# Kernel tuning notes

Hardware: AMD Instinct MI355X
Metric: run time of the kernel (lower is better)

The kernel has to match this reference:

```python
import jax, jax.numpy as jnp
import numpy as np

D_MODEL = 512
NHEAD = 8
D_HEAD = D_MODEL // NHEAD
SCALE = D_HEAD ** -0.5
EPS = 1e-8


def setup_inputs() -> dict:
    key = jax.random.key(0)
    ks = jax.random.split(key, 12)
    B, N = 4, 2048
    s = D_MODEL ** -0.5
    return {
        "Q_input": jax.random.normal(ks[0], (B, N, D_MODEL), jnp.float32),
        "KV_input": jax.random.normal(ks[1], (B, N, D_MODEL), jnp.float32),
        "SC": jax.random.uniform(ks[2], (B, N, N), jnp.float32),
        "Wq_w": jax.random.normal(ks[3], (D_MODEL, D_MODEL), jnp.float32) * s,
        "Wq_b": jnp.zeros((D_MODEL,), jnp.float32),
        "Wk_w": jax.random.normal(ks[4], (D_MODEL, D_MODEL), jnp.float32) * s,
        "Wk_b": jnp.zeros((D_MODEL,), jnp.float32),
        "Wv_w": jax.random.normal(ks[5], (D_MODEL, D_MODEL), jnp.float32) * s,
        "Wv_b": jnp.zeros((D_MODEL,), jnp.float32),
        "gate_w": jax.random.normal(ks[6], (), jnp.float32),
        "gate_b": jnp.zeros((), jnp.float32),
        "out_w": jax.random.normal(ks[7], (D_MODEL, D_MODEL), jnp.float32) * s,
        "out_b": jnp.zeros((D_MODEL,), jnp.float32),
    }


def reference(Q_input, KV_input, SC, Wq_w, Wq_b, Wk_w, Wk_b, Wv_w, Wv_b,
              gate_w, gate_b, out_w, out_b):
    B, N, _ = Q_input.shape
    # projections -> [B, H, N, d_head]
    def proj(x, w, b):
        y = x @ w.T + b
        return y.reshape(B, N, NHEAD, D_HEAD).transpose(0, 2, 1, 3)
    Q = proj(Q_input, Wq_w, Wq_b)
    K = proj(KV_input, Wk_w, Wk_b)
    V = proj(KV_input, Wv_w, Wv_b)
    # scores [B, H, N, N]
    scores = jnp.einsum('bhqd,bhkd->bhqk', Q, K) * SCALE
    # per-edge gate: sigmoid(w*SC + b), broadcast over heads
    g = jax.nn.sigmoid(SC * gate_w + gate_b)  # [B, N, N]
    scores = scores + jnp.log(g + EPS)[:, None, :, :]
    attn = jax.nn.softmax(scores, axis=-1)
    out = jnp.einsum('bhqk,bhkd->bhqd', attn, V)
    out = out.transpose(0, 2, 1, 3).reshape(B, N, D_MODEL)
    return out @ out_w.T + out_b
```

## Files before the change

kernel.cpp:

```cpp
#include <hip/hip_runtime.h>

typedef unsigned short u16;
typedef unsigned int u32;
typedef __attribute__((ext_vector_type(4))) float f32x4;
typedef __attribute__((ext_vector_type(8))) short s16x8;
typedef __attribute__((ext_vector_type(4))) u16 u16x4;

#define L2E 1.4426950408889634f
#define QSCALE 0.18033688011112042f

__device__ __forceinline__ float bf2f(u16 u) {
    union { u32 i; float f; } v; v.i = ((u32)u) << 16; return v.f;
}
__device__ __forceinline__ u16 f2bf(float f) {
    union { float f; u32 i; } v; v.f = f;
    return (u16)((v.i + 0x7fffu + ((v.i >> 16) & 1u)) >> 16);
}
__device__ __forceinline__ u32 pack_hi(float a, float b) {
    union { float f; u32 i; } x, y; x.f = a; y.f = b;
    return (x.i >> 16) | (y.i & 0xFFFF0000u);
}

__device__ __forceinline__ void gl2lds16(const u16* g, u16* l) {
    __builtin_amdgcn_global_load_lds(
        (const __attribute__((address_space(1))) void*)g,
        (__attribute__((address_space(3))) void*)l, 16, 0, 0);
}

__global__ __launch_bounds__(256) void prep_kernel(
    const float* __restrict__ s0, const float* __restrict__ s1,
    const float* __restrict__ s2, const float* __restrict__ s3,
    const float* __restrict__ s4, const float* __restrict__ s5,
    u16* __restrict__ dst,
    const float* __restrict__ SC, const float* __restrict__ gwp,
    const float* __restrict__ gbp, u16* __restrict__ LGx)
{
    if (blockIdx.x < 9216) {
        int e = (blockIdx.x * 256 + threadIdx.x) * 4;
        const float* src; int off;
        if      (e < 4194304) { src = s0; off = e; }
        else if (e < 8388608) { src = s1; off = e - 4194304; }
        else if (e < 8650752) { src = s2; off = e - 8388608; }
        else if (e < 8912896) { src = s3; off = e - 8650752; }
        else if (e < 9175040) { src = s4; off = e - 8912896; }
        else                  { src = s5; off = e - 9175040; }
        f32x4 f = *(const f32x4*)(src + off);
        u16x4 o;
#pragma unroll
        for (int j = 0; j < 4; ++j) o[j] = f2bf(f[j]);
        *(u16x4*)(dst + e) = o;
    } else {
        const int flat = (blockIdx.x - 9216) * 256 + threadIdx.x;
        const int lane = flat & 63;
        const int kt   = (flat >> 6) & 31;
        const int t16  = (flat >> 11) & 127;
        const int b    = flat >> 18;
        const int l16 = lane & 15, quad = lane >> 4;
        const float tA = -gwp[0] * L2E, tB = -gbp[0] * L2E;
        const float* row = SC + ((size_t)b * 2048 + t16 * 16 + l16) * 2048
                              + kt * 64 + quad * 4;
        __align__(16) u16 tmp[16];
#pragma unroll
        for (int kk = 0; kk < 4; ++kk) {
            f32x4 x = *(const f32x4*)(row + kk * 16);
#pragma unroll
            for (int reg = 0; reg < 4; ++reg) {
                float g = __builtin_amdgcn_rcpf(
                    1.0f + __builtin_amdgcn_exp2f(tA * x[reg] + tB)) + 1e-8f;
                tmp[kk * 4 + reg] = f2bf(__builtin_amdgcn_logf(g));
            }
        }
        u16* d = LGx + (size_t)flat * 16;
        *(uint4*)d       = *(uint4*)tmp;
        *(uint4*)(d + 8) = *(uint4*)(tmp + 8);
    }
}

__device__ __forceinline__ void gemm_core(
    const u16* __restrict__ A, const u16* __restrict__ Bw,
    int m0, int n0, u16* As, u16* Bs, f32x4 acc[4][4])
{
    const int tid = threadIdx.x;
    const int lane = tid & 63, w = tid >> 6;
    const int wm = w >> 1, wn = w & 1;
    const int l16 = lane & 15, quad = lane >> 4;
    const int srow = (lane >> 2), sch = (lane & 3) * 8;
    const f32x4 vzero = {0.f, 0.f, 0.f, 0.f};
#pragma unroll
    for (int i = 0; i < 4; ++i)
#pragma unroll
        for (int j = 0; j < 4; ++j) acc[i][j] = vzero;

#pragma unroll
    for (int j = 0; j < 2; ++j) {
        int row = w * 32 + j * 16 + srow;
        gl2lds16(&A[(size_t)(m0 + row) * 512 + sch], &As[w * 1024 + j * 512]);
        gl2lds16(&Bw[(size_t)(n0 + row) * 512 + sch], &Bs[w * 1024 + j * 512]);
    }
    for (int kt = 0; kt < 16; ++kt) {
        __syncthreads();
        const int cur = (kt & 1) * 4096;
        if (kt < 15) {
            const int nxt = ((kt + 1) & 1) * 4096;
#pragma unroll
            for (int j = 0; j < 2; ++j) {
                int row = w * 32 + j * 16 + srow;
                gl2lds16(&A[(size_t)(m0 + row) * 512 + (kt + 1) * 32 + sch],
                         &As[nxt + w * 1024 + j * 512]);
                gl2lds16(&Bw[(size_t)(n0 + row) * 512 + (kt + 1) * 32 + sch],
                         &Bs[nxt + w * 1024 + j * 512]);
            }
        }
        s16x8 af[4], bfr[4];
#pragma unroll
        for (int mt = 0; mt < 4; ++mt)
            af[mt] = *(const s16x8*)&As[cur + (wm * 64 + mt * 16 + l16) * 32 + quad * 8];
#pragma unroll
        for (int nt = 0; nt < 4; ++nt)
            bfr[nt] = *(const s16x8*)&Bs[cur + (wn * 64 + nt * 16 + l16) * 32 + quad * 8];
#pragma unroll
        for (int mt = 0; mt < 4; ++mt)
#pragma unroll
            for (int nt = 0; nt < 4; ++nt)
                acc[mt][nt] = __builtin_amdgcn_mfma_f32_16x16x32_bf16(
                    af[mt], bfr[nt], acc[mt][nt], 0, 0, 0);
    }
}

__global__ __launch_bounds__(256) void proj_kernel(
    const u16* __restrict__ cQin, const u16* __restrict__ cKV,
    const u16* __restrict__ cW,
    const float* __restrict__ bq, const float* __restrict__ bk,
    const float* __restrict__ bv,
    u16* __restrict__ Qh, u16* __restrict__ Kh, u16* __restrict__ Vt)
{
    __shared__ __align__(16) u16 As[2 * 4096];
    __shared__ __align__(16) u16 Bs[2 * 4096];
    const int job = blockIdx.z;
    const u16* A = (job == 0) ? cQin : cKV;
    const u16* W = cW + (size_t)job * 262144;
    const float* bias = (job == 0) ? bq : (job == 1 ? bk : bv);
    const int m0 = blockIdx.y * 128, n0 = blockIdx.x * 128;
    f32x4 acc[4][4];
    gemm_core(A, W, m0, n0, As, Bs, acc);

    const int tid = threadIdx.x, lane = tid & 63, w = tid >> 6;
    const int wm = w >> 1, wn = w & 1, l16 = lane & 15, quad = lane >> 4;
#pragma unroll
    for (int nt = 0; nt < 4; ++nt) {
        int j = n0 + wn * 64 + nt * 16 + l16;
        float bj = bias[j];
        int h = j >> 6, d = j & 63;
#pragma unroll
        for (int mt = 0; mt < 4; ++mt) {
            int trow = m0 + wm * 64 + mt * 16 + quad * 4;
            int bb = trow >> 11, nn = trow & 2047;
            int bh = bb * 8 + h;
            if (job == 2) {
                u16x4 pv;
#pragma unroll
                for (int reg = 0; reg < 4; ++reg) pv[reg] = f2bf(acc[mt][nt][reg] + bj);
                *(u16x4*)&Vt[(size_t)(bh * 64 + d) * 2048 + nn] = pv;
            } else if (job == 0) {
#pragma unroll
                for (int reg = 0; reg < 4; ++reg)
                    Qh[(size_t)(bh * 2048 + nn + reg) * 64 + d] =
                        f2bf((acc[mt][nt][reg] + bj) * QSCALE);
            } else {
#pragma unroll
                for (int reg = 0; reg < 4; ++reg)
                    Kh[(size_t)(bh * 2048 + nn + reg) * 64 + d] =
                        f2bf(acc[mt][nt][reg] + bj);
            }
        }
    }
}

__global__ __launch_bounds__(512, 4) void attn_kernel(
    const u16* __restrict__ Qh, const u16* __restrict__ Kh,
    const u16* __restrict__ Vt, const u16* __restrict__ LGx,
    u16* __restrict__ Ob)
{
    __shared__ __align__(16) u16 Ks[2][4096];
    __shared__ __align__(16) u16 Vs[2][4096];
    __shared__ __align__(16) u16 Plds[8][16][68];
    const int tid = threadIdx.x;
    const int w = tid >> 6, lane = tid & 63;
    const int l16 = lane & 15, quad = lane >> 4;
    const int b = blockIdx.z, head = blockIdx.y, qg = blockIdx.x;
    const int bh = b * 8 + head;
    const int q0 = qg * 128 + w * 16;
    const int t16 = qg * 8 + w;
    const u16* Qp = Qh + (size_t)bh * 131072;
    const u16* Kp = Kh + (size_t)bh * 131072;
    const u16* Vp = Vt + (size_t)bh * 131072;
    const u16* LGt = LGx + ((size_t)((b * 128 + t16) * 32) * 64 + lane) * 16;
    const f32x4 vzero = {0.f, 0.f, 0.f, 0.f};
    const s16x8 ones = {0x3F80, 0x3F80, 0x3F80, 0x3F80,
                        0x3F80, 0x3F80, 0x3F80, 0x3F80};

    const int sr = lane >> 3;
    const int scw = ((lane & 7) ^ sr) * 8;
    const int slab = (w & 3) * 16;
    const bool isK = (w < 4);
    const u16* sG0 = isK ? (Kp + (size_t)(slab + sr) * 64 + scw)
                         : (Vp + (size_t)(slab + sr) * 2048 + scw);
    const u16* sG1 = isK ? (Kp + (size_t)(slab + 8 + sr) * 64 + scw)
                         : (Vp + (size_t)(slab + 8 + sr) * 2048 + scw);
    const size_t sAdv = isK ? 4096 : 64;
    u16* sL0 = isK ? &Ks[0][slab * 64] : &Vs[0][slab * 64];
    u16* sL1 = isK ? &Ks[0][(slab + 8) * 64] : &Vs[0][(slab + 8) * 64];

    s16x8 qf[2];
#pragma unroll
    for (int kc = 0; kc < 2; ++kc)
        qf[kc] = *(const s16x8*)&Qp[(size_t)(q0 + l16) * 64 + kc * 32 + quad * 8];
    f32x4 o[4], lacc = vzero;
#pragma unroll
    for (int dn = 0; dn < 4; ++dn) o[dn] = vzero;

    gl2lds16(sG0, sL0);
    gl2lds16(sG1, sL1);

    for (int kt = 0; kt < 32; ++kt) {
        __syncthreads();
        const int cur = kt & 1;
        if (kt < 31) {
            const int nxt = cur ^ 1;
            gl2lds16(sG0 + (size_t)(kt + 1) * sAdv, sL0 + nxt * 4096);
            gl2lds16(sG1 + (size_t)(kt + 1) * sAdv, sL1 + nxt * 4096);
        }
        const u16* Kb = &Ks[cur][0];
        const u16* Vb = &Vs[cur][0];
        __align__(16) u16 lgv[16];
        *(uint4*)lgv       = *(const uint4*)(LGt + (size_t)kt * 1024);
        *(uint4*)(lgv + 8) = *(const uint4*)(LGt + (size_t)kt * 1024 + 8);

        f32x4 st[4];
#pragma unroll
        for (int kc = 0; kc < 2; ++kc) {
            s16x8 kf[4];
#pragma unroll
            for (int kk = 0; kk < 4; ++kk)
                kf[kk] = *(const s16x8*)&Kb[(kk * 16 + l16) * 64 +
                                            ((kc * 4 + quad) ^ (l16 & 7)) * 8];
#pragma unroll
            for (int kk = 0; kk < 4; ++kk)
                st[kk] = __builtin_amdgcn_mfma_f32_16x16x32_bf16(
                    kf[kk], qf[kc], kc == 0 ? vzero : st[kk], 0, 0, 0);
        }
#pragma unroll
        for (int kk = 0; kk < 4; ++kk) {
            float p0 = __builtin_amdgcn_exp2f(st[kk][0] + bf2f(lgv[kk * 4 + 0]));
            float p1 = __builtin_amdgcn_exp2f(st[kk][1] + bf2f(lgv[kk * 4 + 1]));
            float p2 = __builtin_amdgcn_exp2f(st[kk][2] + bf2f(lgv[kk * 4 + 2]));
            float p3 = __builtin_amdgcn_exp2f(st[kk][3] + bf2f(lgv[kk * 4 + 3]));
            uint2 pk = {pack_hi(p0, p1), pack_hi(p2, p3)};
            *(uint2*)&Plds[w][l16][kk * 16 + quad * 4] = pk;
        }
#pragma unroll
        for (int kc = 0; kc < 2; ++kc) {
            s16x8 pf = *(const s16x8*)&Plds[w][l16][kc * 32 + quad * 8];
            lacc = __builtin_amdgcn_mfma_f32_16x16x32_bf16(pf, ones, lacc, 0, 0, 0);
            s16x8 vf[4];
#pragma unroll
            for (int dn = 0; dn < 4; ++dn)
                vf[dn] = *(const s16x8*)&Vb[(dn * 16 + l16) * 64 +
                                            ((kc * 4 + quad) ^ (l16 & 7)) * 8];
#pragma unroll
            for (int dn = 0; dn < 4; ++dn)
                o[dn] = __builtin_amdgcn_mfma_f32_16x16x32_bf16(
                    pf, vf[dn], o[dn], 0, 0, 0);
        }
    }
#pragma unroll
    for (int reg = 0; reg < 4; ++reg) {
        float inv = __builtin_amdgcn_rcpf(lacc[reg]);
        int trow = b * 2048 + q0 + quad * 4 + reg;
#pragma unroll
        for (int dn = 0; dn < 4; ++dn)
            Ob[(size_t)trow * 512 + head * 64 + dn * 16 + l16] =
                f2bf(o[dn][reg] * inv);
    }
}

__global__ __launch_bounds__(256) void out_kernel(
    const u16* __restrict__ Ob, const u16* __restrict__ cWo,
    const float* __restrict__ bo, float* __restrict__ out)
{
    __shared__ __align__(16) u16 As[2 * 4096];
    __shared__ __align__(16) u16 Bs[2 * 4096];
    const int m0 = blockIdx.y * 128, n0 = blockIdx.x * 128;
    f32x4 acc[4][4];
    gemm_core(Ob, cWo, m0, n0, As, Bs, acc);
    const int tid = threadIdx.x, lane = tid & 63, w = tid >> 6;
    const int wm = w >> 1, wn = w & 1, l16 = lane & 15, quad = lane >> 4;
#pragma unroll
    for (int nt = 0; nt < 4; ++nt) {
        int j = n0 + wn * 64 + nt * 16 + l16;
        float bj = bo[j];
#pragma unroll
        for (int mt = 0; mt < 4; ++mt) {
            int t = m0 + wm * 64 + mt * 16 + quad * 4;
#pragma unroll
            for (int reg = 0; reg < 4; ++reg)
                out[(size_t)(t + reg) * 512 + j] = acc[mt][nt][reg] + bj;
        }
    }
}

extern "C" void kernel_launch(void* const* d_in, const int* in_sizes, int n_in,
                              void* d_out, int out_size, void* d_ws, size_t ws_size,
                              hipStream_t stream)
{
    const float* Qin  = (const float*)d_in[0];
    const float* KVin = (const float*)d_in[1];
    const float* SC   = (const float*)d_in[2];
    const float* Wq   = (const float*)d_in[3];
    const float* bq   = (const float*)d_in[4];
    const float* Wk   = (const float*)d_in[5];
    const float* bk   = (const float*)d_in[6];
    const float* Wv   = (const float*)d_in[7];
    const float* bv   = (const float*)d_in[8];
    const float* gw   = (const float*)d_in[9];
    const float* gb   = (const float*)d_in[10];
    const float* Wo   = (const float*)d_in[11];
    const float* bo   = (const float*)d_in[12];
    float* out = (float*)d_out;

    u16* conv = (u16*)d_ws;
    u16* cQin = conv;
    u16* cKV  = conv + 4194304;
    u16* cW   = conv + 8388608;
    u16* Qh   = conv + 9437184;
    u16* Kh   = Qh + 4194304;
    u16* Vt   = Kh + 4194304;
    u16* Ob   = Vt + 4194304;
    u16* LGx  = Ob + 4194304;

    hipLaunchKernelGGL(prep_kernel, dim3(13312), dim3(256), 0, stream,
                       Qin, KVin, Wq, Wk, Wv, Wo, conv, SC, gw, gb, LGx);
    hipLaunchKernelGGL(proj_kernel, dim3(4, 64, 3), dim3(256), 0, stream,
                       cQin, cKV, cW, bq, bk, bv, Qh, Kh, Vt);
    hipLaunchKernelGGL(attn_kernel, dim3(16, 8, 4), dim3(512), 0, stream,
                       Qh, Kh, Vt, LGx, Ob);
    hipLaunchKernelGGL(out_kernel, dim3(4, 64), dim3(256), 0, stream,
                       Ob, cW + 786432, bo, out);
}
```

Baseline: 244.1 us.

## Switch attention to 32x32x16 MFMA with fragment-major Q/K/V/gate layouts

The attention kernel now uses 32x32x16 bf16 MFMA tiles, with each wave handling 32 query rows instead of 16, so the grid halves to 8 query groups. The projection kernel writes Q, K and V, and the prep kernel writes the log-gate, in a fragment-major layout. Each lane can then load its MFMA operand with one contiguous 16-byte read, and K/V tiles are copied into LDS without swizzling. This aims to cut LDS address arithmetic and bank conflicts and to raise MFMA efficiency. In exchange it uses more accumulator registers, drops the occupancy hint from launch bounds, launches fewer blocks, and makes the projection stores scattered.

New measurement: 255.3 us. 4.6% more time.

```diff
diff --git a/kernel.cpp b/kernel.cpp
--- a/kernel.cpp
+++ b/kernel.cpp
@@ -3,6 +3,7 @@
 typedef unsigned short u16;
 typedef unsigned int u32;
 typedef __attribute__((ext_vector_type(4))) float f32x4;
+typedef __attribute__((ext_vector_type(16))) float f32x16;
 typedef __attribute__((ext_vector_type(8))) short s16x8;
 typedef __attribute__((ext_vector_type(4))) u16 u16x4;
 
@@ -20,7 +21,6 @@
     union { float f; u32 i; } x, y; x.f = a; y.f = b;
     return (x.i >> 16) | (y.i & 0xFFFF0000u);
 }
-
 __device__ __forceinline__ void gl2lds16(const u16* g, u16* l) {
     __builtin_amdgcn_global_load_lds(
         (const __attribute__((address_space(1))) void*)g,
@@ -52,22 +52,23 @@
     } else {
         const int flat = (blockIdx.x - 9216) * 256 + threadIdx.x;
         const int lane = flat & 63;
-        const int kt   = (flat >> 6) & 31;
-        const int t16  = (flat >> 11) & 127;
+        const int ks   = (flat >> 6) & 1;
+        const int kt   = (flat >> 7) & 31;
+        const int qt   = (flat >> 12) & 63;
         const int b    = flat >> 18;
-        const int l16 = lane & 15, quad = lane >> 4;
+        const int l31 = lane & 31, hl = lane >> 5;
         const float tA = -gwp[0] * L2E, tB = -gbp[0] * L2E;
-        const float* row = SC + ((size_t)b * 2048 + t16 * 16 + l16) * 2048
-                              + kt * 64 + quad * 4;
+        const float* row = SC + ((size_t)b * 2048 + qt * 32 + l31) * 2048
+                              + kt * 64 + ks * 32 + 4 * hl;
         __align__(16) u16 tmp[16];
 #pragma unroll
-        for (int kk = 0; kk < 4; ++kk) {
-            f32x4 x = *(const f32x4*)(row + kk * 16);
-#pragma unroll
-            for (int reg = 0; reg < 4; ++reg) {
+        for (int rg = 0; rg < 4; ++rg) {
+            f32x4 x = *(const f32x4*)(row + rg * 8);
+#pragma unroll
+            for (int i = 0; i < 4; ++i) {
                 float g = __builtin_amdgcn_rcpf(
-                    1.0f + __builtin_amdgcn_exp2f(tA * x[reg] + tB)) + 1e-8f;
-                tmp[kk * 4 + reg] = f2bf(__builtin_amdgcn_logf(g));
+                    1.0f + __builtin_amdgcn_exp2f(tA * x[i] + tB)) + 1e-8f;
+                tmp[rg * 4 + i] = f2bf(__builtin_amdgcn_logf(g));
             }
         }
         u16* d = LGx + (size_t)flat * 16;
@@ -132,7 +133,7 @@
     const u16* __restrict__ cW,
     const float* __restrict__ bq, const float* __restrict__ bk,
     const float* __restrict__ bv,
-    u16* __restrict__ Qh, u16* __restrict__ Kh, u16* __restrict__ Vt)
+    u16* __restrict__ Qh, u16* __restrict__ Kh, u16* __restrict__ Vh)
 {
     __shared__ __align__(16) u16 As[2 * 4096];
     __shared__ __align__(16) u16 Bs[2 * 4096];
@@ -148,139 +149,139 @@
     const int wm = w >> 1, wn = w & 1, l16 = lane & 15, quad = lane >> 4;
 #pragma unroll
     for (int nt = 0; nt < 4; ++nt) {
-        int j = n0 + wn * 64 + nt * 16 + l16;
-        float bj = bias[j];
-        int h = j >> 6, d = j & 63;
+        int feat = n0 + wn * 64 + nt * 16 + l16;
+        float bj = bias[feat];
+        int h = feat >> 6, d = feat & 63;
 #pragma unroll
         for (int mt = 0; mt < 4; ++mt) {
-            int trow = m0 + wm * 64 + mt * 16 + quad * 4;
-            int bb = trow >> 11, nn = trow & 2047;
+            int token = m0 + wm * 64 + mt * 16 + quad * 4;
+            int bb = token >> 11, nn = token & 2047;
             int bh = bb * 8 + h;
             if (job == 2) {
+                int kt = nn >> 6, kk = (nn >> 4) & 3;
+                int hl2 = (nn >> 3) & 1, jj = nn & 7;
+                int ds = d >> 5, d31 = d & 31;
+                size_t idx = ((((size_t)bh * 32 + kt) * 8 + ds * 4 + kk) * 64 +
+                              32 * hl2 + d31) * 8 + jj;
                 u16x4 pv;
 #pragma unroll
                 for (int reg = 0; reg < 4; ++reg) pv[reg] = f2bf(acc[mt][nt][reg] + bj);
-                *(u16x4*)&Vt[(size_t)(bh * 64 + d) * 2048 + nn] = pv;
+                *(u16x4*)&Vh[idx] = pv;
             } else if (job == 0) {
-#pragma unroll
-                for (int reg = 0; reg < 4; ++reg)
-                    Qh[(size_t)(bh * 2048 + nn + reg) * 64 + d] =
-                        f2bf((acc[mt][nt][reg] + bj) * QSCALE);
+                int dd = d >> 4, hl = (d >> 3) & 1, j = d & 7;
+#pragma unroll
+                for (int reg = 0; reg < 4; ++reg) {
+                    int q = nn + reg;
+                    size_t idx = ((((size_t)bh * 64 + (q >> 5)) * 4 + dd) * 64 +
+                                  32 * hl + (q & 31)) * 8 + j;
+                    Qh[idx] = f2bf((acc[mt][nt][reg] + bj) * QSCALE);
+                }
             } else {
-#pragma unroll
-                for (int reg = 0; reg < 4; ++reg)
-                    Kh[(size_t)(bh * 2048 + nn + reg) * 64 + d] =
-                        f2bf(acc[mt][nt][reg] + bj);
-            }
-        }
-    }
-}
-
-__global__ __launch_bounds__(512, 4) void attn_kernel(
+                int dd = d >> 4, hl = (d >> 3) & 1, j = d & 7;
+#pragma unroll
+                for (int reg = 0; reg < 4; ++reg) {
+                    int key = nn + reg;
+                    size_t idx = ((((size_t)bh * 32 + (key >> 6)) * 8 +
+                                   ((key >> 5) & 1) * 4 + dd) * 64 +
+                                  32 * hl + (key & 31)) * 8 + j;
+                    Kh[idx] = f2bf(acc[mt][nt][reg] + bj);
+                }
+            }
+        }
+    }
+}
+
+__global__ __launch_bounds__(512) void attn_kernel(
     const u16* __restrict__ Qh, const u16* __restrict__ Kh,
-    const u16* __restrict__ Vt, const u16* __restrict__ LGx,
+    const u16* __restrict__ Vh, const u16* __restrict__ LGx,
     u16* __restrict__ Ob)
 {
     __shared__ __align__(16) u16 Ks[2][4096];
     __shared__ __align__(16) u16 Vs[2][4096];
-    __shared__ __align__(16) u16 Plds[8][16][68];
+    __shared__ __align__(16) u16 Pl[8 * 2048];
     const int tid = threadIdx.x;
     const int w = tid >> 6, lane = tid & 63;
-    const int l16 = lane & 15, quad = lane >> 4;
+    const int l31 = lane & 31, hl = lane >> 5;
     const int b = blockIdx.z, head = blockIdx.y, qg = blockIdx.x;
     const int bh = b * 8 + head;
-    const int q0 = qg * 128 + w * 16;
-    const int t16 = qg * 8 + w;
-    const u16* Qp = Qh + (size_t)bh * 131072;
-    const u16* Kp = Kh + (size_t)bh * 131072;
-    const u16* Vp = Vt + (size_t)bh * 131072;
-    const u16* LGt = LGx + ((size_t)((b * 128 + t16) * 32) * 64 + lane) * 16;
-    const f32x4 vzero = {0.f, 0.f, 0.f, 0.f};
+    const int qt = qg * 8 + w, q0 = qt * 32;
+    const u16* Qp = Qh + ((size_t)bh * 64 + qt) * 2048;
+    const u16* Kbase = Kh + (size_t)bh * 131072;
+    const u16* Vbase = Vh + (size_t)bh * 131072;
+    const u16* LGt = LGx + (((size_t)(b * 64 + qt)) * 64) * 1024;
     const s16x8 ones = {0x3F80, 0x3F80, 0x3F80, 0x3F80,
                         0x3F80, 0x3F80, 0x3F80, 0x3F80};
-
-    const int sr = lane >> 3;
-    const int scw = ((lane & 7) ^ sr) * 8;
-    const int slab = (w & 3) * 16;
-    const bool isK = (w < 4);
-    const u16* sG0 = isK ? (Kp + (size_t)(slab + sr) * 64 + scw)
-                         : (Vp + (size_t)(slab + sr) * 2048 + scw);
-    const u16* sG1 = isK ? (Kp + (size_t)(slab + 8 + sr) * 64 + scw)
-                         : (Vp + (size_t)(slab + 8 + sr) * 2048 + scw);
-    const size_t sAdv = isK ? 4096 : 64;
-    u16* sL0 = isK ? &Ks[0][slab * 64] : &Vs[0][slab * 64];
-    u16* sL1 = isK ? &Ks[0][(slab + 8) * 64] : &Vs[0][(slab + 8) * 64];
-
-    s16x8 qf[2];
-#pragma unroll
-    for (int kc = 0; kc < 2; ++kc)
-        qf[kc] = *(const s16x8*)&Qp[(size_t)(q0 + l16) * 64 + kc * 32 + quad * 8];
-    f32x4 o[4], lacc = vzero;
-#pragma unroll
-    for (int dn = 0; dn < 4; ++dn) o[dn] = vzero;
-
-    gl2lds16(sG0, sL0);
-    gl2lds16(sG1, sL1);
+    const f32x16 z16 = {};
+
+    s16x8 qf[4];
+#pragma unroll
+    for (int dd = 0; dd < 4; ++dd)
+        qf[dd] = *(const s16x8*)&Qp[dd * 512 + lane * 8];
+    f32x16 o0 = z16, o1 = z16, lacc = z16;
+
+    gl2lds16(Kbase + w * 512 + lane * 8, &Ks[0][w * 512]);
+    gl2lds16(Vbase + w * 512 + lane * 8, &Vs[0][w * 512]);
 
     for (int kt = 0; kt < 32; ++kt) {
         __syncthreads();
         const int cur = kt & 1;
         if (kt < 31) {
             const int nxt = cur ^ 1;
-            gl2lds16(sG0 + (size_t)(kt + 1) * sAdv, sL0 + nxt * 4096);
-            gl2lds16(sG1 + (size_t)(kt + 1) * sAdv, sL1 + nxt * 4096);
+            gl2lds16(Kbase + (size_t)(kt + 1) * 4096 + w * 512 + lane * 8,
+                     &Ks[nxt][w * 512]);
+            gl2lds16(Vbase + (size_t)(kt + 1) * 4096 + w * 512 + lane * 8,
+                     &Vs[nxt][w * 512]);
         }
         const u16* Kb = &Ks[cur][0];
         const u16* Vb = &Vs[cur][0];
-        __align__(16) u16 lgv[16];
-        *(uint4*)lgv       = *(const uint4*)(LGt + (size_t)kt * 1024);
-        *(uint4*)(lgv + 8) = *(const uint4*)(LGt + (size_t)kt * 1024 + 8);
-
-        f32x4 st[4];
-#pragma unroll
-        for (int kc = 0; kc < 2; ++kc) {
-            s16x8 kf[4];
-#pragma unroll
-            for (int kk = 0; kk < 4; ++kk)
-                kf[kk] = *(const s16x8*)&Kb[(kk * 16 + l16) * 64 +
-                                            ((kc * 4 + quad) ^ (l16 & 7)) * 8];
-#pragma unroll
-            for (int kk = 0; kk < 4; ++kk)
-                st[kk] = __builtin_amdgcn_mfma_f32_16x16x32_bf16(
-                    kf[kk], qf[kc], kc == 0 ? vzero : st[kk], 0, 0, 0);
+
+        f32x16 st[2];
+#pragma unroll
+        for (int ks = 0; ks < 2; ++ks) {
+            st[ks] = z16;
+#pragma unroll
+            for (int dd = 0; dd < 4; ++dd) {
+                s16x8 kf = *(const s16x8*)&Kb[(ks * 4 + dd) * 512 + lane * 8];
+                st[ks] = __builtin_amdgcn_mfma_f32_32x32x16_bf16(
+                    kf, qf[dd], st[ks], 0, 0, 0);
+            }
+        }
+#pragma unroll
+        for (int ks = 0; ks < 2; ++ks) {
+            __align__(16) u16 lgv[16];
+            const u16* lgp = LGt + (size_t)(kt * 2 + ks) * 1024 + lane * 16;
+            *(uint4*)lgv       = *(const uint4*)lgp;
+            *(uint4*)(lgv + 8) = *(const uint4*)(lgp + 8);
+#pragma unroll
+            for (int rg = 0; rg < 4; ++rg) {
+                const int r = rg * 4;
+                float p0 = __builtin_amdgcn_exp2f(st[ks][r + 0] + bf2f(lgv[r + 0]));
+                float p1 = __builtin_amdgcn_exp2f(st[ks][r + 1] + bf2f(lgv[r + 1]));
+                float p2 = __builtin_amdgcn_exp2f(st[ks][r + 2] + bf2f(lgv[r + 2]));
+                float p3 = __builtin_amdgcn_exp2f(st[ks][r + 3] + bf2f(lgv[r + 3]));
+                uint2 pk = {pack_hi(p0, p1), pack_hi(p2, p3)};
+                const int key0 = ks * 32 + rg * 8 + 4 * hl;
+                const int kk = key0 >> 4, hla = (key0 >> 3) & 1, j0 = key0 & 7;
+                *(uint2*)&Pl[w * 2048 + kk * 512 + (32 * hla + l31) * 8 + j0] = pk;
+            }
         }
 #pragma unroll
         for (int kk = 0; kk < 4; ++kk) {
-            float p0 = __builtin_amdgcn_exp2f(st[kk][0] + bf2f(lgv[kk * 4 + 0]));
-            float p1 = __builtin_amdgcn_exp2f(st[kk][1] + bf2f(lgv[kk * 4 + 1]));
-            float p2 = __builtin_amdgcn_exp2f(st[kk][2] + bf2f(lgv[kk * 4 + 2]));
-            float p3 = __builtin_amdgcn_exp2f(st[kk][3] + bf2f(lgv[kk * 4 + 3]));
-            uint2 pk = {pack_hi(p0, p1), pack_hi(p2, p3)};
-            *(uint2*)&Plds[w][l16][kk * 16 + quad * 4] = pk;
-        }
-#pragma unroll
-        for (int kc = 0; kc < 2; ++kc) {
-            s16x8 pf = *(const s16x8*)&Plds[w][l16][kc * 32 + quad * 8];
-            lacc = __builtin_amdgcn_mfma_f32_16x16x32_bf16(pf, ones, lacc, 0, 0, 0);
-            s16x8 vf[4];
-#pragma unroll
-            for (int dn = 0; dn < 4; ++dn)
-                vf[dn] = *(const s16x8*)&Vb[(dn * 16 + l16) * 64 +
-                                            ((kc * 4 + quad) ^ (l16 & 7)) * 8];
-#pragma unroll
-            for (int dn = 0; dn < 4; ++dn)
-                o[dn] = __builtin_amdgcn_mfma_f32_16x16x32_bf16(
-                    pf, vf[dn], o[dn], 0, 0, 0);
-        }
-    }
-#pragma unroll
-    for (int reg = 0; reg < 4; ++reg) {
+            s16x8 pf = *(const s16x8*)&Pl[w * 2048 + kk * 512 + lane * 8];
+            lacc = __builtin_amdgcn_mfma_f32_32x32x16_bf16(pf, ones, lacc, 0, 0, 0);
+            s16x8 vf0 = *(const s16x8*)&Vb[(0 * 4 + kk) * 512 + lane * 8];
+            s16x8 vf1 = *(const s16x8*)&Vb[(1 * 4 + kk) * 512 + lane * 8];
+            o0 = __builtin_amdgcn_mfma_f32_32x32x16_bf16(pf, vf0, o0, 0, 0, 0);
+            o1 = __builtin_amdgcn_mfma_f32_32x32x16_bf16(pf, vf1, o1, 0, 0, 0);
+        }
+    }
+#pragma unroll
+    for (int reg = 0; reg < 16; ++reg) {
+        const int qrow = (reg & 3) + 8 * (reg >> 2) + 4 * hl;
         float inv = __builtin_amdgcn_rcpf(lacc[reg]);
-        int trow = b * 2048 + q0 + quad * 4 + reg;
-#pragma unroll
-        for (int dn = 0; dn < 4; ++dn)
-            Ob[(size_t)trow * 512 + head * 64 + dn * 16 + l16] =
-                f2bf(o[dn][reg] * inv);
+        size_t base = ((size_t)(b * 2048 + q0 + qrow)) * 512 + head * 64;
+        Ob[base + l31]      = f2bf(o0[reg] * inv);
+        Ob[base + 32 + l31] = f2bf(o1[reg] * inv);
     }
 }
 
@@ -334,16 +335,16 @@
     u16* cW   = conv + 8388608;
     u16* Qh   = conv + 9437184;
     u16* Kh   = Qh + 4194304;
-    u16* Vt   = Kh + 4194304;
-    u16* Ob   = Vt + 4194304;
+    u16* Vh   = Kh + 4194304;
+    u16* Ob   = Vh + 4194304;
     u16* LGx  = Ob + 4194304;
 
     hipLaunchKernelGGL(prep_kernel, dim3(13312), dim3(256), 0, stream,
                        Qin, KVin, Wq, Wk, Wv, Wo, conv, SC, gw, gb, LGx);
     hipLaunchKernelGGL(proj_kernel, dim3(4, 64, 3), dim3(256), 0, stream,
-                       cQin, cKV, cW, bq, bk, bv, Qh, Kh, Vt);
-    hipLaunchKernelGGL(attn_kernel, dim3(16, 8, 4), dim3(512), 0, stream,
-                       Qh, Kh, Vt, LGx, Ob);
+                       cQin, cKV, cW, bq, bk, bv, Qh, Kh, Vh);
+    hipLaunchKernelGGL(attn_kernel, dim3(8, 8, 4), dim3(512), 0, stream,
+                       Qh, Kh, Vh, LGx, Ob);
     hipLaunchKernelGGL(out_kernel, dim3(4, 64), dim3(256), 0, stream,
                        Ob, cW + 786432, bo, out);
 }
```
